# Optimization experiments

Hardware: AMD Instinct MI355X
Metric: run time of the kernel (lower is better)

Reference implementation:

```python
import jax, jax.numpy as jnp
import numpy as np

EMBED = 1024
HEADS = 16
HEAD_DIM = EMBED // HEADS
B, L = 4, 2048


def setup_inputs() -> dict:
    key = jax.random.key(0)
    ks = jax.random.split(key, 10)
    s = 1.0 / np.sqrt(EMBED)
    x = jax.random.normal(ks[0], (B, L, EMBED), dtype=jnp.float32)
    mask = jax.random.randint(ks[1], (B, 1, L, L), 0, 2, dtype=jnp.int32)
    Wq = jax.random.normal(ks[2], (EMBED, EMBED), dtype=jnp.float32) * s
    Wk = jax.random.normal(ks[3], (EMBED, EMBED), dtype=jnp.float32) * s
    Wv = jax.random.normal(ks[4], (EMBED, EMBED), dtype=jnp.float32) * s
    Wo = jax.random.normal(ks[5], (EMBED, EMBED), dtype=jnp.float32) * s
    bq = jnp.zeros((EMBED,), jnp.float32)
    bk = jnp.zeros((EMBED,), jnp.float32)
    bv = jnp.zeros((EMBED,), jnp.float32)
    bo = jnp.zeros((EMBED,), jnp.float32)
    return {"x": x, "mask": mask, "Wq": Wq, "bq": bq, "Wk": Wk, "bk": bk,
            "Wv": Wv, "bv": bv, "Wo": Wo, "bo": bo}


def reference(x, mask, Wq, bq, Wk, bk, Wv, bv, Wo, bo):
    n, l, _ = x.shape
    q = (x @ Wq + bq).reshape(n, l, HEADS, HEAD_DIM)
    k = (x @ Wk + bk).reshape(n, l, HEADS, HEAD_DIM)
    v = (x @ Wv + bv).reshape(n, l, HEADS, HEAD_DIM)
    # [n, h, q, k] scores
    energy = jnp.einsum('nqhd,nkhd->nhqk', q, k)
    energy = jnp.where(mask == 0, jnp.float32(-1e20), energy)
    attn = jax.nn.softmax(energy / jnp.sqrt(jnp.float32(HEAD_DIM)), axis=-1)
    out = jnp.einsum('nhqk,nkhd->nqhd', attn, v).reshape(n, l, EMBED)
    return out @ Wo + bo
```

## Files before the change

### kernel.cpp

```cpp
#include <hip/hip_runtime.h>
#include <hip/hip_bf16.h>

#define EMBED 1024
#define HEADS 16
#define HDIM 64
#define BATCH 4
#define SEQ 2048
#define ROWS (BATCH * SEQ)
#define LOG2E 1.4426950408889634f

typedef __attribute__((ext_vector_type(8))) short bf16x8;
typedef __attribute__((ext_vector_type(4))) float f32x4;

#define MFMA16(a, b, c) __builtin_amdgcn_mfma_f32_16x16x32_bf16(a, b, c, 0, 0, 0)

__device__ __forceinline__ unsigned short f2bf(float f) {
    union { float f; unsigned int u; } x; x.f = f;
    unsigned int r = x.u + 0x7fffu + ((x.u >> 16) & 1u);
    return (unsigned short)(r >> 16);
}

__device__ __forceinline__ unsigned int pkbf(float a, float b) {
#if __has_builtin(__builtin_amdgcn_cvt_pk_bf16_f32)
    auto v = __builtin_amdgcn_cvt_pk_bf16_f32(a, b);
    unsigned int u; __builtin_memcpy(&u, &v, 4); return u;
#else
    union { __hip_bfloat162 h; unsigned int u; } c;
    c.h = __float22bfloat162_rn(make_float2(a, b)); return c.u;
#endif
}

__device__ __forceinline__ void gl2lds(const unsigned short* g, unsigned short* l) {
    __builtin_amdgcn_global_load_lds(
        (const __attribute__((address_space(1))) unsigned int*)g,
        (__attribute__((address_space(3))) unsigned int*)l, 16, 0, 0);
}

__global__ __launch_bounds__(256) void cvt_x_kernel(
    const float* __restrict__ in, unsigned short* __restrict__ out)
{
    int i = (blockIdx.x * 256 + threadIdx.x) * 4;
    float4 v = *(const float4*)(in + i);
    uint2 o; o.x = pkbf(v.x, v.y); o.y = pkbf(v.z, v.w);
    *(uint2*)(out + i) = o;
}

__global__ __launch_bounds__(256) void wtrans_kernel(
    const float* __restrict__ W0, const float* __restrict__ W1,
    const float* __restrict__ W2, const float* __restrict__ W3,
    unsigned short* __restrict__ Wt)
{
    __shared__ float t[32][33];
    const float* W = (blockIdx.z == 0) ? W0 : (blockIdx.z == 1) ? W1
                   : (blockIdx.z == 2) ? W2 : W3;
    unsigned short* o = Wt + (size_t)blockIdx.z * EMBED * EMBED;
    int tx = threadIdx.x & 31, ty = threadIdx.x >> 5;
    int bx = blockIdx.x * 32, by = blockIdx.y * 32;
#pragma unroll
    for (int r = 0; r < 32; r += 8)
        t[ty + r][tx] = W[(size_t)(by + ty + r) * EMBED + bx + tx];
    __syncthreads();
#pragma unroll
    for (int r = 0; r < 32; r += 8)
        o[(size_t)(bx + ty + r) * EMBED + by + tx] = f2bf(t[tx][ty + r]);
}

__global__ __launch_bounds__(256) void cvt_mask_kernel(
    const int* __restrict__ in, unsigned char* __restrict__ out)
{
    int i = (blockIdx.x * 256 + threadIdx.x) * 4;
    int4 v = *(const int4*)(in + i);
    uchar4 o;
    o.x = v.x ? 0xFF : 0; o.y = v.y ? 0xFF : 0;
    o.z = v.z ? 0xFF : 0; o.w = v.w ? 0xFF : 0;
    *(uchar4*)(out + i) = o;
}

__device__ __forceinline__ void gemm_bf16_body(
    const unsigned short* __restrict__ A, const unsigned short* __restrict__ Bt,
    const float* __restrict__ bias,
    float* __restrict__ outF, unsigned short* __restrict__ outB, float scale,
    int vmode)
{
    __shared__ unsigned short As[128][32];
    __shared__ unsigned short Bs[128][32];
    const int tid = threadIdx.x;
    const int lane = tid & 63, wid = tid >> 6;
    const int ln = lane & 15, lg = lane >> 4;
    const int wy = wid >> 1, wx = wid & 1;
    const int m0 = blockIdx.y * 128, n0 = blockIdx.x * 128;
    const int srow = tid >> 2;
    const int scol = (((tid & 3) ^ ((tid >> 2) & 3) ^ ((tid >> 4) & 3)) << 3);
    const unsigned short* Ap = A + (size_t)(m0 + srow) * EMBED + scol;
    const unsigned short* Bp = Bt + (size_t)(n0 + srow) * EMBED + scol;
    unsigned short* lA = &As[srow & ~15][0];
    unsigned short* lB = &Bs[srow & ~15][0];
    const int swg = ((lg ^ (ln & 3) ^ (ln >> 2)) << 3);

    f32x4 acc[4][4];
#pragma unroll
    for (int i = 0; i < 4; i++)
#pragma unroll
        for (int j = 0; j < 4; j++) acc[i][j] = (f32x4){0.f, 0.f, 0.f, 0.f};

    for (int k0 = 0; k0 < EMBED; k0 += 32) {
        __syncthreads();
        gl2lds(Ap + k0, lA);
        gl2lds(Ap + (size_t)64 * EMBED + k0, lA + 64 * 32);
        gl2lds(Bp + k0, lB);
        gl2lds(Bp + (size_t)64 * EMBED + k0, lB + 64 * 32);
        __syncthreads();
        bf16x8 af[4], bfr[4];
#pragma unroll
        for (int mi = 0; mi < 4; mi++)
            af[mi] = *(const bf16x8*)&As[wy * 64 + mi * 16 + ln][swg];
#pragma unroll
        for (int nj = 0; nj < 4; nj++)
            bfr[nj] = *(const bf16x8*)&Bs[wx * 64 + nj * 16 + ln][swg];
#pragma unroll
        for (int mi = 0; mi < 4; mi++)
#pragma unroll
            for (int nj = 0; nj < 4; nj++)
                acc[mi][nj] = MFMA16(af[mi], bfr[nj], acc[mi][nj]);
    }

#pragma unroll
    for (int mi = 0; mi < 4; mi++) {
#pragma unroll
        for (int nj = 0; nj < 4; nj++) {
            int row = m0 + wy * 64 + mi * 16 + lg * 4;
            int col = n0 + wx * 64 + nj * 16 + ln;
            float bv = bias[col];
            if (vmode) {
                int bb = row >> 11, s = row & (SEQ - 1);
                int hh = col >> 6, dd = col & 63;
                unsigned short* dst = outB +
                    ((size_t)((bb * HEADS + hh) * HDIM + dd)) * SEQ + s;
                uint2 pw;
                pw.x = pkbf(acc[mi][nj][0] + bv, acc[mi][nj][1] + bv);
                pw.y = pkbf(acc[mi][nj][2] + bv, acc[mi][nj][3] + bv);
                *(uint2*)dst = pw;
            } else {
#pragma unroll
                for (int r = 0; r < 4; r++) {
                    float v = (acc[mi][nj][r] + bv) * scale;
                    if (outF) outF[(size_t)(row + r) * EMBED + col] = v;
                    else      outB[(size_t)(row + r) * EMBED + col] = f2bf(v);
                }
            }
        }
    }
}

__global__ __launch_bounds__(256) void qkv_gemm_kernel(
    const unsigned short* __restrict__ Xb, const unsigned short* __restrict__ Wt,
    const float* __restrict__ bq, const float* __restrict__ bk,
    const float* __restrict__ bv,
    unsigned short* __restrict__ Qb, unsigned short* __restrict__ Kb,
    unsigned short* __restrict__ Vt)
{
    int z = blockIdx.z;
    const unsigned short* Bt = Wt + (size_t)z * EMBED * EMBED;
    const float* bias = (z == 0) ? bq : (z == 1) ? bk : bv;
    unsigned short* out = (z == 0) ? Qb : (z == 1) ? Kb : Vt;
    float scale = (z == 0) ? 0.125f * LOG2E : 1.0f;
    gemm_bf16_body(Xb, Bt, bias, nullptr, out, scale, z == 2);
}

__global__ __launch_bounds__(256) void out_gemm_kernel(
    const unsigned short* __restrict__ Ob, const unsigned short* __restrict__ Wto,
    const float* __restrict__ bo, float* __restrict__ out)
{
    gemm_bf16_body(Ob, Wto, bo, out, nullptr, 1.0f, 0);
}

__global__ __launch_bounds__(256) void attn_mfma_kernel(
    const unsigned short* __restrict__ Qb, const unsigned short* __restrict__ Kb,
    const unsigned short* __restrict__ Vt, const unsigned char* __restrict__ mask8,
    unsigned short* __restrict__ Ob)
{
    __shared__ unsigned short Ks[2][64][64];
    __shared__ unsigned short Vs[2][64][64];
    __shared__ unsigned short Ps[4][32][64];
    const int tid = threadIdx.x;
    const int lane = tid & 63, wid = tid >> 6;
    const int ln = lane & 15, lg = lane >> 4;
    const int b = blockIdx.z, h = blockIdx.y;
    const int q0 = blockIdx.x * 128 + wid * 32;

    bf16x8 qf[2][2];
#pragma unroll
    for (int mi = 0; mi < 2; mi++)
#pragma unroll
        for (int ks = 0; ks < 2; ks++)
            qf[mi][ks] = *(const bf16x8*)(Qb +
                (size_t)(b * SEQ + q0 + mi * 16 + ln) * EMBED + h * HDIM + ks * 32 + lg * 8);

    bf16x8 ones;
#pragma unroll
    for (int i = 0; i < 8; i++) ones[i] = (short)0x3F80;

    f32x4 o[2][4];
#pragma unroll
    for (int mi = 0; mi < 2; mi++)
#pragma unroll
        for (int dj = 0; dj < 4; dj++) o[mi][dj] = (f32x4){0.f, 0.f, 0.f, 0.f};
    f32x4 lacc[2] = {(f32x4){0.f, 0.f, 0.f, 0.f}, (f32x4){0.f, 0.f, 0.f, 0.f}};

    const int srow = tid >> 3;
    const int scolKV = (((tid & 7) ^ ((tid >> 3) & 7)) << 3);
    const unsigned short* Kp = Kb + (size_t)(b * SEQ + srow) * EMBED + h * HDIM + scolKV;
    const unsigned short* Vp = Vt + (size_t)((b * HEADS + h) * HDIM + srow) * SEQ + scolKV;
    unsigned short* lK[2] = {&Ks[0][srow & ~7][0], &Ks[1][srow & ~7][0]};
    unsigned short* lV[2] = {&Vs[0][srow & ~7][0], &Vs[1][srow & ~7][0]};

    const unsigned char* mq0 = mask8 + (size_t)b * SEQ * SEQ + (size_t)(q0 + ln) * SEQ;
    const unsigned char* mq1 = mq0 + (size_t)16 * SEQ;

    const int swk = ((lg ^ (ln & 7)) << 3);

    int pwr[4], prd[2];
#pragma unroll
    for (int nj = 0; nj < 4; nj++)
        pwr[nj] = (((2 * nj + (lg >> 1)) ^ (ln & 7)) << 3) + ((lg & 1) << 2);
#pragma unroll
    for (int ks = 0; ks < 2; ks++)
        prd[ks] = ((4 * ks + lg) ^ (ln & 7)) << 3;
    unsigned short* ps0 = &Ps[wid][ln][0];
    unsigned short* ps1 = &Ps[wid][16 + ln][0];

    gl2lds(Kp, lK[0]);
    gl2lds(Kp + (size_t)32 * EMBED, lK[0] + 32 * 64);
    gl2lds(Vp, lV[0]);
    gl2lds(Vp + (size_t)32 * SEQ, lV[0] + 32 * 64);

    const int NT = SEQ / 64;
    for (int t = 0; t < NT; t++) {
        const int cur = t & 1;
        const int kt = t * 64;
        __syncthreads();

        unsigned int mw[2][4];
#pragma unroll
        for (int mi = 0; mi < 2; mi++) {
            const unsigned char* mq = (mi ? mq1 : mq0) + kt;
#pragma unroll
            for (int nj = 0; nj < 4; nj++)
                mw[mi][nj] = *(const unsigned int*)(mq + nj * 16 + lg * 4);
        }

        if (t + 1 < NT) {
            const int nk = kt + 64;
            gl2lds(Kp + (size_t)nk * EMBED, lK[cur ^ 1]);
            gl2lds(Kp + (size_t)(nk + 32) * EMBED, lK[cur ^ 1] + 32 * 64);
            gl2lds(Vp + nk, lV[cur ^ 1]);
            gl2lds(Vp + (size_t)(32 * SEQ) + nk, lV[cur ^ 1] + 32 * 64);
        }

        f32x4 S[2][4];
#pragma unroll
        for (int nj = 0; nj < 4; nj++) {
            bf16x8 k0 = *(const bf16x8*)&Ks[cur][nj * 16 + ln][swk];
            bf16x8 k1 = *(const bf16x8*)&Ks[cur][nj * 16 + ln][swk ^ 32];
#pragma unroll
            for (int mi = 0; mi < 2; mi++) {
                f32x4 t2 = (f32x4){0.f, 0.f, 0.f, 0.f};
                t2 = MFMA16(k0, qf[mi][0], t2);
                t2 = MFMA16(k1, qf[mi][1], t2);
                S[mi][nj] = t2;
            }
        }

#pragma unroll
        for (int mi = 0; mi < 2; mi++) {
            unsigned short* psb = mi ? ps1 : ps0;
#pragma unroll
            for (int nj = 0; nj < 4; nj++) {
                float p0 = __builtin_amdgcn_exp2f(S[mi][nj][0]);
                float p1 = __builtin_amdgcn_exp2f(S[mi][nj][1]);
                float p2 = __builtin_amdgcn_exp2f(S[mi][nj][2]);
                float p3 = __builtin_amdgcn_exp2f(S[mi][nj][3]);
                unsigned int m = mw[mi][nj];
                unsigned int d0 = __builtin_amdgcn_perm(0u, m, 0x01010000u);
                unsigned int d1 = __builtin_amdgcn_perm(0u, m, 0x03030202u);
                uint2 pw;
                pw.x = pkbf(p0, p1) & d0;
                pw.y = pkbf(p2, p3) & d1;
                *(uint2*)(psb + pwr[nj]) = pw;
            }
        }

#pragma unroll
        for (int ks = 0; ks < 2; ks++) {
            bf16x8 p0 = *(const bf16x8*)(ps0 + prd[ks]);
            bf16x8 p1 = *(const bf16x8*)(ps1 + prd[ks]);
            lacc[0] = MFMA16(p0, ones, lacc[0]);
            lacc[1] = MFMA16(p1, ones, lacc[1]);
#pragma unroll
            for (int dj = 0; dj < 4; dj++) {
                bf16x8 vf = *(const bf16x8*)&Vs[cur][dj * 16 + ln][swk ^ (ks << 5)];
                o[0][dj] = MFMA16(p0, vf, o[0][dj]);
                o[1][dj] = MFMA16(p1, vf, o[1][dj]);
            }
        }
    }

#pragma unroll
    for (int mi = 0; mi < 2; mi++) {
        float l0 = 1.0f / lacc[mi][0];
        float l1 = 1.0f / lacc[mi][1];
        float l2 = 1.0f / lacc[mi][2];
        float l3 = 1.0f / lacc[mi][3];
#pragma unroll
        for (int dj = 0; dj < 4; dj++) {
            unsigned short* op = Ob + (size_t)(b * SEQ + q0 + mi * 16 + lg * 4) * EMBED
                                    + h * HDIM + dj * 16 + ln;
            op[0]         = f2bf(o[mi][dj][0] * l0);
            op[EMBED]     = f2bf(o[mi][dj][1] * l1);
            op[2 * EMBED] = f2bf(o[mi][dj][2] * l2);
            op[3 * EMBED] = f2bf(o[mi][dj][3] * l3);
        }
    }
}

extern "C" void kernel_launch(void* const* d_in, const int* in_sizes, int n_in,
                              void* d_out, int out_size, void* d_ws, size_t ws_size,
                              hipStream_t stream)
{
    const float* x  = (const float*)d_in[0];
    const int* mask = (const int*)d_in[1];
    const float* Wq = (const float*)d_in[2];
    const float* bq = (const float*)d_in[3];
    const float* Wk = (const float*)d_in[4];
    const float* bk = (const float*)d_in[5];
    const float* Wv = (const float*)d_in[6];
    const float* bv = (const float*)d_in[7];
    const float* Wo = (const float*)d_in[8];
    const float* bo = (const float*)d_in[9];
    float* outp = (float*)d_out;

    char* ws = (char*)d_ws;
    unsigned short* Wt = (unsigned short*)(ws);
    unsigned char*  m8 = (unsigned char*)(ws + ((size_t)8 << 20));
    unsigned short* Xb = (unsigned short*)(ws + ((size_t)24 << 20));
    unsigned short* Ob = Xb;
    unsigned short* Qb = (unsigned short*)(ws + ((size_t)40 << 20));
    unsigned short* Kb = (unsigned short*)(ws + ((size_t)56 << 20));
    unsigned short* Vt = (unsigned short*)(ws + ((size_t)72 << 20));

    cvt_x_kernel<<<ROWS * EMBED / 1024, 256, 0, stream>>>(x, Xb);
    wtrans_kernel<<<dim3(32, 32, 4), 256, 0, stream>>>(Wq, Wk, Wv, Wo, Wt);
    cvt_mask_kernel<<<(size_t)BATCH * SEQ * SEQ / 1024, 256, 0, stream>>>(mask, m8);
    qkv_gemm_kernel<<<dim3(EMBED / 128, ROWS / 128, 3), 256, 0, stream>>>(
        Xb, Wt, bq, bk, bv, Qb, Kb, Vt);
    attn_mfma_kernel<<<dim3(SEQ / 128, HEADS, BATCH), 256, 0, stream>>>(
        Qb, Kb, Vt, m8, Ob);
    out_gemm_kernel<<<dim3(EMBED / 128, ROWS / 128), 256, 0, stream>>>(
        Ob, Wt + (size_t)3 * EMBED * EMBED, bo, outp);
}
```

Measured before the change: 427.8 us.

## Merge prep kernels, widen GEMM K-tile, drop attention KV double buffering

Folds the three preprocessing kernels (x to bf16, mask to bytes, weight transpose) into one launch dispatched by block index, which cuts launch overhead. The shared GEMM body now stages a 64-wide K slice per iteration with a new XOR swizzle, halving the number of barriers per tile. The attention kernel drops its double-buffered K/V prefetch in favour of a single buffer loaded synchronously each step. That shrinks LDS use, possibly raising occupancy, but it exposes load latency that the prefetch used to hide.

```diff
diff --git a/kernel.cpp b/kernel.cpp
--- a/kernel.cpp
+++ b/kernel.cpp
@@ -36,44 +36,46 @@
         (__attribute__((address_space(3))) unsigned int*)l, 16, 0, 0);
 }
 
-__global__ __launch_bounds__(256) void cvt_x_kernel(
-    const float* __restrict__ in, unsigned short* __restrict__ out)
-{
-    int i = (blockIdx.x * 256 + threadIdx.x) * 4;
-    float4 v = *(const float4*)(in + i);
-    uint2 o; o.x = pkbf(v.x, v.y); o.y = pkbf(v.z, v.w);
-    *(uint2*)(out + i) = o;
-}
-
-__global__ __launch_bounds__(256) void wtrans_kernel(
+#define XBLK 8192
+#define MBLK 16384
+#define WBLK 4096
+
+__global__ __launch_bounds__(256) void prep_kernel(
+    const float* __restrict__ x, const int* __restrict__ mask,
     const float* __restrict__ W0, const float* __restrict__ W1,
     const float* __restrict__ W2, const float* __restrict__ W3,
+    unsigned short* __restrict__ Xb, unsigned char* __restrict__ m8,
     unsigned short* __restrict__ Wt)
 {
     __shared__ float t[32][33];
-    const float* W = (blockIdx.z == 0) ? W0 : (blockIdx.z == 1) ? W1
-                   : (blockIdx.z == 2) ? W2 : W3;
-    unsigned short* o = Wt + (size_t)blockIdx.z * EMBED * EMBED;
-    int tx = threadIdx.x & 31, ty = threadIdx.x >> 5;
-    int bx = blockIdx.x * 32, by = blockIdx.y * 32;
-#pragma unroll
-    for (int r = 0; r < 32; r += 8)
-        t[ty + r][tx] = W[(size_t)(by + ty + r) * EMBED + bx + tx];
-    __syncthreads();
-#pragma unroll
-    for (int r = 0; r < 32; r += 8)
-        o[(size_t)(bx + ty + r) * EMBED + by + tx] = f2bf(t[tx][ty + r]);
-}
-
-__global__ __launch_bounds__(256) void cvt_mask_kernel(
-    const int* __restrict__ in, unsigned char* __restrict__ out)
-{
-    int i = (blockIdx.x * 256 + threadIdx.x) * 4;
-    int4 v = *(const int4*)(in + i);
-    uchar4 o;
-    o.x = v.x ? 0xFF : 0; o.y = v.y ? 0xFF : 0;
-    o.z = v.z ? 0xFF : 0; o.w = v.w ? 0xFF : 0;
-    *(uchar4*)(out + i) = o;
+    const int bid = blockIdx.x;
+    if (bid < XBLK) {
+        int i = (bid * 256 + threadIdx.x) * 4;
+        float4 v = *(const float4*)(x + i);
+        uint2 o; o.x = pkbf(v.x, v.y); o.y = pkbf(v.z, v.w);
+        *(uint2*)(Xb + i) = o;
+    } else if (bid < XBLK + MBLK) {
+        int i = ((bid - XBLK) * 256 + threadIdx.x) * 4;
+        int4 v = *(const int4*)(mask + i);
+        uchar4 o;
+        o.x = v.x ? 0xFF : 0; o.y = v.y ? 0xFF : 0;
+        o.z = v.z ? 0xFF : 0; o.w = v.w ? 0xFF : 0;
+        *(uchar4*)(m8 + i) = o;
+    } else {
+        int f = bid - XBLK - MBLK;
+        int z = f >> 10, rem = f & 1023;
+        const float* W = (z == 0) ? W0 : (z == 1) ? W1 : (z == 2) ? W2 : W3;
+        unsigned short* o = Wt + (size_t)z * EMBED * EMBED;
+        int tx = threadIdx.x & 31, ty = threadIdx.x >> 5;
+        int bx = (rem & 31) * 32, by = (rem >> 5) * 32;
+#pragma unroll
+        for (int r = 0; r < 32; r += 8)
+            t[ty + r][tx] = W[(size_t)(by + ty + r) * EMBED + bx + tx];
+        __syncthreads();
+#pragma unroll
+        for (int r = 0; r < 32; r += 8)
+            o[(size_t)(bx + ty + r) * EMBED + by + tx] = f2bf(t[tx][ty + r]);
+    }
 }
 
 __device__ __forceinline__ void gemm_bf16_body(
@@ -82,20 +84,19 @@
     float* __restrict__ outF, unsigned short* __restrict__ outB, float scale,
     int vmode)
 {
-    __shared__ unsigned short As[128][32];
-    __shared__ unsigned short Bs[128][32];
+    __shared__ unsigned short As[128][64];
+    __shared__ unsigned short Bs[128][64];
     const int tid = threadIdx.x;
     const int lane = tid & 63, wid = tid >> 6;
     const int ln = lane & 15, lg = lane >> 4;
     const int wy = wid >> 1, wx = wid & 1;
     const int m0 = blockIdx.y * 128, n0 = blockIdx.x * 128;
-    const int srow = tid >> 2;
-    const int scol = (((tid & 3) ^ ((tid >> 2) & 3) ^ ((tid >> 4) & 3)) << 3);
-    const unsigned short* Ap = A + (size_t)(m0 + srow) * EMBED + scol;
-    const unsigned short* Bp = Bt + (size_t)(n0 + srow) * EMBED + scol;
-    unsigned short* lA = &As[srow & ~15][0];
-    unsigned short* lB = &Bs[srow & ~15][0];
-    const int swg = ((lg ^ (ln & 3) ^ (ln >> 2)) << 3);
+    const int r0 = wid * 32 + (lane >> 3);
+    const int scol = (((lane & 7) ^ ((lane >> 3) & 7)) << 3);
+    const unsigned short* Ap = A + (size_t)(m0 + r0) * EMBED + scol;
+    const unsigned short* Bp = Bt + (size_t)(n0 + r0) * EMBED + scol;
+    unsigned short* lA = &As[wid * 32][0];
+    unsigned short* lB = &Bs[wid * 32][0];
 
     f32x4 acc[4][4];
 #pragma unroll
@@ -103,25 +104,33 @@
 #pragma unroll
         for (int j = 0; j < 4; j++) acc[i][j] = (f32x4){0.f, 0.f, 0.f, 0.f};
 
-    for (int k0 = 0; k0 < EMBED; k0 += 32) {
-        __syncthreads();
-        gl2lds(Ap + k0, lA);
-        gl2lds(Ap + (size_t)64 * EMBED + k0, lA + 64 * 32);
-        gl2lds(Bp + k0, lB);
-        gl2lds(Bp + (size_t)64 * EMBED + k0, lB + 64 * 32);
-        __syncthreads();
-        bf16x8 af[4], bfr[4];
-#pragma unroll
-        for (int mi = 0; mi < 4; mi++)
-            af[mi] = *(const bf16x8*)&As[wy * 64 + mi * 16 + ln][swg];
-#pragma unroll
-        for (int nj = 0; nj < 4; nj++)
-            bfr[nj] = *(const bf16x8*)&Bs[wx * 64 + nj * 16 + ln][swg];
-#pragma unroll
-        for (int mi = 0; mi < 4; mi++)
+    for (int k0 = 0; k0 < EMBED; k0 += 64) {
+        __syncthreads();
+#pragma unroll
+        for (int is = 0; is < 4; is++) {
+            gl2lds(Ap + k0 + (size_t)(is * 8) * EMBED, lA + is * 8 * 64);
+            gl2lds(Bp + k0 + (size_t)(is * 8) * EMBED, lB + is * 8 * 64);
+        }
+        __syncthreads();
+        bf16x8 af[2][4], bfr[2][4];
+#pragma unroll
+        for (int s = 0; s < 2; s++) {
+#pragma unroll
+            for (int mi = 0; mi < 4; mi++)
+                af[s][mi] = *(const bf16x8*)
+                    &As[wy * 64 + mi * 16 + ln][(((lg + 4 * s) ^ (ln & 7)) << 3)];
 #pragma unroll
             for (int nj = 0; nj < 4; nj++)
-                acc[mi][nj] = MFMA16(af[mi], bfr[nj], acc[mi][nj]);
+                bfr[s][nj] = *(const bf16x8*)
+                    &Bs[wx * 64 + nj * 16 + ln][(((lg + 4 * s) ^ (ln & 7)) << 3)];
+        }
+#pragma unroll
+        for (int s = 0; s < 2; s++)
+#pragma unroll
+            for (int mi = 0; mi < 4; mi++)
+#pragma unroll
+                for (int nj = 0; nj < 4; nj++)
+                    acc[mi][nj] = MFMA16(af[s][mi], bfr[s][nj], acc[mi][nj]);
     }
 
 #pragma unroll
@@ -179,8 +188,8 @@
     const unsigned short* __restrict__ Vt, const unsigned char* __restrict__ mask8,
     unsigned short* __restrict__ Ob)
 {
-    __shared__ unsigned short Ks[2][64][64];
-    __shared__ unsigned short Vs[2][64][64];
+    __shared__ unsigned short Ks[64][64];
+    __shared__ unsigned short Vs[64][64];
     __shared__ unsigned short Ps[4][32][64];
     const int tid = threadIdx.x;
     const int lane = tid & 63, wid = tid >> 6;
@@ -211,8 +220,8 @@
     const int scolKV = (((tid & 7) ^ ((tid >> 3) & 7)) << 3);
     const unsigned short* Kp = Kb + (size_t)(b * SEQ + srow) * EMBED + h * HDIM + scolKV;
     const unsigned short* Vp = Vt + (size_t)((b * HEADS + h) * HDIM + srow) * SEQ + scolKV;
-    unsigned short* lK[2] = {&Ks[0][srow & ~7][0], &Ks[1][srow & ~7][0]};
-    unsigned short* lV[2] = {&Vs[0][srow & ~7][0], &Vs[1][srow & ~7][0]};
+    unsigned short* lK = &Ks[srow & ~7][0];
+    unsigned short* lV = &Vs[srow & ~7][0];
 
     const unsigned char* mq0 = mask8 + (size_t)b * SEQ * SEQ + (size_t)(q0 + ln) * SEQ;
     const unsigned char* mq1 = mq0 + (size_t)16 * SEQ;
@@ -229,17 +238,7 @@
     unsigned short* ps0 = &Ps[wid][ln][0];
     unsigned short* ps1 = &Ps[wid][16 + ln][0];
 
-    gl2lds(Kp, lK[0]);
-    gl2lds(Kp + (size_t)32 * EMBED, lK[0] + 32 * 64);
-    gl2lds(Vp, lV[0]);
-    gl2lds(Vp + (size_t)32 * SEQ, lV[0] + 32 * 64);
-
-    const int NT = SEQ / 64;
-    for (int t = 0; t < NT; t++) {
-        const int cur = t & 1;
-        const int kt = t * 64;
-        __syncthreads();
-
+    for (int kt = 0; kt < SEQ; kt += 64) {
         unsigned int mw[2][4];
 #pragma unroll
         for (int mi = 0; mi < 2; mi++) {
@@ -249,19 +248,18 @@
                 mw[mi][nj] = *(const unsigned int*)(mq + nj * 16 + lg * 4);
         }
 
-        if (t + 1 < NT) {
-            const int nk = kt + 64;
-            gl2lds(Kp + (size_t)nk * EMBED, lK[cur ^ 1]);
-            gl2lds(Kp + (size_t)(nk + 32) * EMBED, lK[cur ^ 1] + 32 * 64);
-            gl2lds(Vp + nk, lV[cur ^ 1]);
-            gl2lds(Vp + (size_t)(32 * SEQ) + nk, lV[cur ^ 1] + 32 * 64);
-        }
+        __syncthreads();
+        gl2lds(Kp + (size_t)kt * EMBED, lK);
+        gl2lds(Kp + (size_t)(kt + 32) * EMBED, lK + 32 * 64);
+        gl2lds(Vp + kt, lV);
+        gl2lds(Vp + (size_t)32 * SEQ + kt, lV + 32 * 64);
+        __syncthreads();
 
         f32x4 S[2][4];
 #pragma unroll
         for (int nj = 0; nj < 4; nj++) {
-            bf16x8 k0 = *(const bf16x8*)&Ks[cur][nj * 16 + ln][swk];
-            bf16x8 k1 = *(const bf16x8*)&Ks[cur][nj * 16 + ln][swk ^ 32];
+            bf16x8 k0 = *(const bf16x8*)&Ks[nj * 16 + ln][swk];
+            bf16x8 k1 = *(const bf16x8*)&Ks[nj * 16 + ln][swk ^ 32];
 #pragma unroll
             for (int mi = 0; mi < 2; mi++) {
                 f32x4 t2 = (f32x4){0.f, 0.f, 0.f, 0.f};
@@ -298,7 +296,7 @@
             lacc[1] = MFMA16(p1, ones, lacc[1]);
 #pragma unroll
             for (int dj = 0; dj < 4; dj++) {
-                bf16x8 vf = *(const bf16x8*)&Vs[cur][dj * 16 + ln][swk ^ (ks << 5)];
+                bf16x8 vf = *(const bf16x8*)&Vs[dj * 16 + ln][swk ^ (ks << 5)];
                 o[0][dj] = MFMA16(p0, vf, o[0][dj]);
                 o[1][dj] = MFMA16(p1, vf, o[1][dj]);
             }
@@ -348,9 +346,8 @@
     unsigned short* Kb = (unsigned short*)(ws + ((size_t)56 << 20));
     unsigned short* Vt = (unsigned short*)(ws + ((size_t)72 << 20));
 
-    cvt_x_kernel<<<ROWS * EMBED / 1024, 256, 0, stream>>>(x, Xb);
-    wtrans_kernel<<<dim3(32, 32, 4), 256, 0, stream>>>(Wq, Wk, Wv, Wo, Wt);
-    cvt_mask_kernel<<<(size_t)BATCH * SEQ * SEQ / 1024, 256, 0, stream>>>(mask, m8);
+    prep_kernel<<<XBLK + MBLK + WBLK, 256, 0, stream>>>(
+        x, mask, Wq, Wk, Wv, Wo, Xb, m8, Wt);
     qkv_gemm_kernel<<<dim3(EMBED / 128, ROWS / 128, 3), 256, 0, stream>>>(
         Xb, Wt, bq, bk, bv, Qb, Kb, Vt);
     attn_mfma_kernel<<<dim3(SEQ / 128, HEADS, BATCH), 256, 0, stream>>>(
```

After: 397.9 us. -7.0%, faster.
